# Kernel optimization log

Hardware: AMD Instinct MI355X
Metric: run time of the kernel (lower is better)

The kernel has to match this reference:

```python
import jax, jax.numpy as jnp
import numpy as np

D_MODEL, D_STATE, D_CONV, EXPAND = 1024, 16, 4, 2
D_INNER = EXPAND * D_MODEL
B, L = 2, 4096
LN_EPS = 1e-5


def setup_inputs() -> dict:
    key = jax.random.key(0)
    ks = jax.random.split(key, 6)
    x = jax.random.normal(ks[0], (B, L, D_MODEL), dtype=jnp.float32)
    ln_gamma = jnp.ones((D_MODEL,), jnp.float32)
    ln_beta = jnp.zeros((D_MODEL,), jnp.float32)
    W_in = jax.random.normal(ks[1], (2 * D_INNER, D_MODEL), jnp.float32) / np.sqrt(D_MODEL).astype(np.float32)
    conv_w = jax.random.normal(ks[2], (D_INNER, 1, D_CONV), jnp.float32) * 0.1
    conv_b = jnp.zeros((D_INNER,), jnp.float32)
    W_out = jax.random.normal(ks[3], (D_MODEL, D_INNER), jnp.float32) / np.sqrt(D_INNER).astype(np.float32)
    A = jnp.eye(D_STATE, dtype=jnp.float32)
    Bm = jax.random.normal(ks[4], (D_STATE, D_INNER), jnp.float32) * 0.01
    Cm = jax.random.normal(ks[5], (D_STATE, D_INNER), jnp.float32) * 0.01
    return dict(x=x, ln_gamma=ln_gamma, ln_beta=ln_beta, W_in=W_in,
                conv_w=conv_w, conv_b=conv_b, W_out=W_out, A=A, Bm=Bm, Cm=Cm)


def _layernorm(x, gamma, beta):
    mu = jnp.mean(x, axis=-1, keepdims=True)
    var = jnp.mean(jnp.square(x - mu), axis=-1, keepdims=True)
    return (x - mu) * jax.lax.rsqrt(var + LN_EPS) * gamma + beta


def _causal_depthwise_conv(xp, conv_w, conv_b):
    # xp: (B, L, D_INNER) -> torch Conv1d(padding=K-1, groups=C) then slice [:L]
    # == left-pad K-1, valid depthwise conv.
    lhs = jnp.pad(xp.transpose(0, 2, 1), ((0, 0), (0, 0), (D_CONV - 1, 0)))  # (B,C,L+K-1)
    out = jax.lax.conv_general_dilated(
        lhs, conv_w, window_strides=(1,), padding='VALID',
        dimension_numbers=('NCH', 'OIH', 'NCH'), feature_group_count=D_INNER)
    return out.transpose(0, 2, 1) + conv_b  # (B, L, C)


def reference(x, ln_gamma, ln_beta, W_in, conv_w, conv_b, W_out, A, Bm, Cm):
    # scan permutation is identity (untrained optimizer state); masking disabled
    xn = _layernorm(x, ln_gamma, ln_beta)
    xz = jnp.einsum('bld,ed->ble', xn, W_in)          # (B, L, 2*D_INNER)
    x_part, z = jnp.split(xz, 2, axis=-1)             # each (B, L, D_INNER)
    x_conv = jax.nn.silu(_causal_depthwise_conv(x_part, conv_w, conv_b))

    # recurrence: s_t = s_{t-1} @ A.T + u_t @ B.T ; out_t = (x_conv_t + s_t @ C) * sigmoid(z_t)
    u_seq = x_part.transpose(1, 0, 2)                 # (L, B, D_INNER)
    xc_seq = x_conv.transpose(1, 0, 2)
    z_seq = z.transpose(1, 0, 2)

    def step(state, inp):
        u_t, xc_t, z_t = inp
        state = state @ A.T + u_t @ Bm.T              # (B, D_STATE)
        out = (xc_t + state @ Cm) * jax.nn.sigmoid(z_t)
        return state, out

    state0 = jnp.zeros((x.shape[0], D_STATE), x.dtype)
    _, ys = jax.lax.scan(step, state0, (u_seq, xc_seq, z_seq))
    y = ys.transpose(1, 0, 2)                         # (B, L, D_INNER)
    residual = jnp.einsum('bli,di->bld', y, W_out)    # (B, L, D_MODEL)
    return x + residual
```

## Files before the change

### kernel.cpp

```cpp
#include <hip/hip_runtime.h>
#include <hip/hip_bf16.h>
#include <math.h>

#define D_MODEL 1024
#define D_STATE 16
#define D_CONV 4
#define D_INNER 2048
#define BATCH 2
#define SEQ 4096
#define NROW (BATCH * SEQ)
#define LN_EPS 1e-5f

typedef __attribute__((ext_vector_type(8))) short  bf16x8_t;
typedef __attribute__((ext_vector_type(4))) float  f32x4_t;
typedef __attribute__((ext_vector_type(8))) unsigned short u16x8_t;

__device__ inline unsigned short f2bf(float f) {
    unsigned u = __float_as_uint(f);
    u += 0x7fffu + ((u >> 16) & 1u);
    return (unsigned short)(u >> 16);
}
__device__ inline float bf2f(unsigned short u) {
    return __uint_as_float((unsigned)u << 16);
}

#define GLL16(g, l)                                                            \
    __builtin_amdgcn_global_load_lds(                                          \
        (const __attribute__((address_space(1))) void*)(g),                    \
        (__attribute__((address_space(3))) void*)(l), 16, 0, 0)

#define FENCE asm volatile("" ::: "memory")
#define BAR do { FENCE; __builtin_amdgcn_s_barrier(); FENCE; } while (0)

#define CVT_BLOCKS 3088
__global__ __launch_bounds__(256) void pre_kernel(const float* __restrict__ x,
                                                  const float* __restrict__ gamma,
                                                  const float* __restrict__ beta,
                                                  const float* __restrict__ W_in,
                                                  const float* __restrict__ W_out,
                                                  const float* __restrict__ Bm,
                                                  unsigned short* __restrict__ xn,
                                                  unsigned short* __restrict__ Win_bf,
                                                  unsigned short* __restrict__ Wout_bf,
                                                  unsigned short* __restrict__ Bm_bf) {
    __shared__ float red[8];
    const int tid = threadIdx.x;
    if (blockIdx.x < CVT_BLOCKS) {
        const long long g = (long long)(blockIdx.x * 256 + tid) * 8;
        const long long n1 = (long long)2 * D_INNER * D_MODEL;
        const long long n2 = n1 + (long long)D_MODEL * D_INNER;
        const float* src; unsigned short* dst; long long off;
        if (g < n1)      { src = W_in;  dst = Win_bf;  off = g; }
        else if (g < n2) { src = W_out; dst = Wout_bf; off = g - n1; }
        else             { src = Bm;    dst = Bm_bf;   off = g - n2; }
        const float4 a = *reinterpret_cast<const float4*>(src + off);
        const float4 b = *reinterpret_cast<const float4*>(src + off + 4);
        u16x8_t p;
        p[0] = f2bf(a.x); p[1] = f2bf(a.y); p[2] = f2bf(a.z); p[3] = f2bf(a.w);
        p[4] = f2bf(b.x); p[5] = f2bf(b.y); p[6] = f2bf(b.z); p[7] = f2bf(b.w);
        *reinterpret_cast<u16x8_t*>(dst + off) = p;
        return;
    }
    const int row = blockIdx.x - CVT_BLOCKS;
    const float4* xr = reinterpret_cast<const float4*>(x + (size_t)row * D_MODEL);
    float4 v = xr[tid];

    const int lane = tid & 63, wave = tid >> 6;
    float s = v.x + v.y + v.z + v.w;
    #pragma unroll
    for (int off = 32; off > 0; off >>= 1) s += __shfl_down(s, off, 64);
    if (lane == 0) red[wave] = s;
    __syncthreads();
    float mu = (red[0] + red[1] + red[2] + red[3]) * (1.0f / D_MODEL);
    __syncthreads();

    float dx = v.x - mu, dy = v.y - mu, dz = v.z - mu, dw = v.w - mu;
    float ss = dx * dx + dy * dy + dz * dz + dw * dw;
    #pragma unroll
    for (int off = 32; off > 0; off >>= 1) ss += __shfl_down(ss, off, 64);
    if (lane == 0) red[wave] = ss;
    __syncthreads();
    float var = (red[0] + red[1] + red[2] + red[3]) * (1.0f / D_MODEL);
    float rs = rsqrtf(var + LN_EPS);

    const float4 gv = reinterpret_cast<const float4*>(gamma)[tid];
    const float4 bv = reinterpret_cast<const float4*>(beta)[tid];
    ushort4 o;
    o.x = f2bf(dx * rs * gv.x + bv.x);
    o.y = f2bf(dy * rs * gv.y + bv.y);
    o.z = f2bf(dz * rs * gv.z + bv.z);
    o.w = f2bf(dw * rs * gv.w + bv.w);
    reinterpret_cast<ushort4*>(xn + (size_t)row * D_MODEL)[tid] = o;
}

__global__ __launch_bounds__(512, 2) void gemm256_bf16(const short* __restrict__ A,
                                                       const short* __restrict__ B,
                                                       unsigned short* __restrict__ Cb,
                                                       int M, int N, int K) {
    __shared__ short lds[2 * 4 * 8192];

    const int tid = threadIdx.x;
    const int w = tid >> 6, l = tid & 63;

    const int id = blockIdx.y * gridDim.x + blockIdx.x;
    const int cpx = (gridDim.x * gridDim.y) >> 3;
    const int sid = (id & 7) * cpx + (id >> 3);
    const int row0 = (sid / gridDim.x) * 256;
    const int col0 = (sid % gridDim.x) * 256;

    const int wm = w >> 2;
    const int wn = w & 3;
    const int fr = l & 15;
    const int fc = (l >> 4) * 8;
    const int NT = K >> 6;

    const int qa = wm;
    const int qb = 2 + (wn >> 1);
    const int bb = (wn & 1) * 64;

    auto STAGE = [&](const short* __restrict__ G, int growbase, int k0,
                     int buf, int q) {
        #pragma unroll
        for (int j = 0; j < 2; ++j) {
            const int e = ((j * 8 + w) << 9) + l * 8;
            const int r = e >> 6;
            const int c = (e & 63) ^ ((r & 7) << 3);
            GLL16(G + (size_t)(growbase + r) * K + k0 + c,
                  &lds[buf * 32768 + q * 8192 + ((j * 8 + w) << 9)]);
        }
    };
    auto LDF = [&](int buf, int q, int r, int ks) -> bf16x8_t {
        const int c = (ks * 32 + fc) ^ ((r & 7) << 3);
        return *reinterpret_cast<const bf16x8_t*>(
            &lds[buf * 32768 + q * 8192 + r * 64 + c]);
    };

    f32x4_t acc[8][4] = {};
    bf16x8_t af[4][2], af2[4][2], bA[2][2], bB[2][2];

#define MFMA_Q(AF, mh, nh, BFR)                                                \
    do {                                                                       \
        _Pragma("unroll")                                                      \
        for (int mi = 0; mi < 4; ++mi)                                         \
            _Pragma("unroll")                                                  \
            for (int ni = 0; ni < 2; ++ni)                                     \
                _Pragma("unroll")                                              \
                for (int ks = 0; ks < 2; ++ks)                                 \
                    acc[(mh) * 4 + mi][(nh) * 2 + ni] =                        \
                        __builtin_amdgcn_mfma_f32_16x16x32_bf16(               \
                            AF[mi][ks], BFR[ni][ks],                           \
                            acc[(mh) * 4 + mi][(nh) * 2 + ni], 0, 0, 0);       \
    } while (0)

    STAGE(A, row0,       0, 0, 0);
    STAGE(A, row0 + 128, 0, 0, 1);
    STAGE(B, col0,       0, 0, 2);
    STAGE(B, col0 + 128, 0, 0, 3);
    if (NT > 1) {
        STAGE(B, col0,       64, 1, 2);
        STAGE(B, col0 + 128, 64, 1, 3);
        STAGE(A, row0,       64, 1, 0);
        asm volatile("s_waitcnt vmcnt(6)" ::: "memory");
    } else {
        asm volatile("s_waitcnt vmcnt(0)" ::: "memory");
    }
    BAR;

    for (int kt = 0; kt < NT; ++kt) {
        const int buf = kt & 1, nbuf = buf ^ 1;
        #pragma unroll
        for (int mi = 0; mi < 4; ++mi)
            #pragma unroll
            for (int ks = 0; ks < 2; ++ks)
                af[mi][ks] = LDF(buf, qa, mi * 16 + fr, ks);
        #pragma unroll
        for (int ni = 0; ni < 2; ++ni)
            #pragma unroll
            for (int ks = 0; ks < 2; ++ks)
                bA[ni][ks] = LDF(buf, qb, bb + ni * 16 + fr, ks);
        #pragma unroll
        for (int ni = 0; ni < 2; ++ni)
            #pragma unroll
            for (int ks = 0; ks < 2; ++ks)
                bB[ni][ks] = LDF(buf, qb, bb + 32 + ni * 16 + fr, ks);
        #pragma unroll
        for (int mi = 0; mi < 4; ++mi)
            #pragma unroll
            for (int ks = 0; ks < 2; ++ks)
                af2[mi][ks] = LDF(buf, qa, 64 + mi * 16 + fr, ks);
        if (kt + 1 < NT) STAGE(A, row0 + 128, (kt + 1) << 6, nbuf, 1);
        asm volatile("s_waitcnt lgkmcnt(0)" ::: "memory");
        BAR;
        if (kt + 2 < NT) {
            STAGE(B, col0,       (kt + 2) << 6, buf, 2);
            STAGE(B, col0 + 128, (kt + 2) << 6, buf, 3);
            STAGE(A, row0,       (kt + 2) << 6, buf, 0);
            asm volatile("s_waitcnt vmcnt(6)" ::: "memory");
        } else {
            asm volatile("s_waitcnt vmcnt(0)" ::: "memory");
        }
        BAR;
        __builtin_amdgcn_s_setprio(1);
        MFMA_Q(af,  0, 0, bA);
        MFMA_Q(af,  0, 1, bB);
        MFMA_Q(af2, 1, 1, bB);
        MFMA_Q(af2, 1, 0, bA);
        __builtin_amdgcn_s_setprio(0);
    }
#undef MFMA_Q

    const int cr = (l >> 4) * 4;
    const int cc = l & 15;
    #pragma unroll
    for (int m = 0; m < 8; ++m) {
        #pragma unroll
        for (int n = 0; n < 4; ++n) {
            size_t base = (size_t)(row0 + wm * 128 + m * 16 + cr) * N +
                          (col0 + wn * 64 + n * 16 + cc);
            #pragma unroll
            for (int j = 0; j < 4; ++j)
                Cb[base + (size_t)j * N] = f2bf(acc[m][n][j]);
        }
    }
}

__global__ __launch_bounds__(512) void gemm_out(const short* __restrict__ A,
                                                const short* __restrict__ B,
                                                const float* __restrict__ add,
                                                float* __restrict__ C,
                                                int M, int N, int K) {
    __shared__ short lds[3 * 3 * 8192];

    const int tid = threadIdx.x;
    const int w = tid >> 6, l = tid & 63;

    const int id = blockIdx.y * gridDim.x + blockIdx.x;
    const int cpx = (gridDim.x * gridDim.y) >> 3;
    const int sid = (id & 7) * cpx + (id >> 3);
    const int row0 = (sid / gridDim.x) * 256;
    const int col0 = (sid % gridDim.x) * 128;

    const int wm = w >> 1;
    const int wn = w & 1;
    const int qa = wm >> 1;
    const int lr0 = (wm & 1) * 64;
    const int fr = l & 15;
    const int fc = (l >> 4) * 8;
    const int NT = K >> 6;

    auto STAGE = [&](const short* __restrict__ G, int growbase, int k0,
                     int buf, int q) {
        #pragma unroll
        for (int j = 0; j < 2; ++j) {
            const int e = ((j * 8 + w) << 9) + l * 8;
            const int r = e >> 6;
            const int c = (e & 63) ^ ((r & 7) << 3);
            GLL16(G + (size_t)(growbase + r) * K + k0 + c,
                  &lds[buf * 24576 + q * 8192 + ((j * 8 + w) << 9)]);
        }
    };
    auto LDF = [&](int buf, int q, int r, int ks) -> bf16x8_t {
        const int c = (ks * 32 + fc) ^ ((r & 7) << 3);
        return *reinterpret_cast<const bf16x8_t*>(
            &lds[buf * 24576 + q * 8192 + r * 64 + c]);
    };

    f32x4_t acc[4][4] = {};
    bf16x8_t af[4][2], bf[4][2];

    STAGE(A, row0,       0, 0, 0);
    STAGE(A, row0 + 128, 0, 0, 1);
    STAGE(B, col0,       0, 0, 2);
    if (NT > 1) {
        STAGE(A, row0,       64, 1, 0);
        STAGE(A, row0 + 128, 64, 1, 1);
        STAGE(B, col0,       64, 1, 2);
        asm volatile("s_waitcnt vmcnt(6)" ::: "memory");
    } else {
        asm volatile("s_waitcnt vmcnt(0)" ::: "memory");
    }

    int buf = 0;
    for (int kt = 0; kt < NT; ++kt) {
        BAR;
        #pragma unroll
        for (int mi = 0; mi < 4; ++mi)
            #pragma unroll
            for (int ks = 0; ks < 2; ++ks)
                af[mi][ks] = LDF(buf, qa, lr0 + mi * 16 + fr, ks);
        #pragma unroll
        for (int ni = 0; ni < 4; ++ni)
            #pragma unroll
            for (int ks = 0; ks < 2; ++ks)
                bf[ni][ks] = LDF(buf, 2, wn * 64 + ni * 16 + fr, ks);
        __builtin_amdgcn_s_setprio(1);
        #pragma unroll
        for (int mi = 0; mi < 4; ++mi)
            #pragma unroll
            for (int ni = 0; ni < 4; ++ni)
                #pragma unroll
                for (int ks = 0; ks < 2; ++ks)
                    acc[mi][ni] = __builtin_amdgcn_mfma_f32_16x16x32_bf16(
                        af[mi][ks], bf[ni][ks], acc[mi][ni], 0, 0, 0);
        __builtin_amdgcn_s_setprio(0);
        if (kt + 2 < NT) {
            const int sb = (buf + 2) % 3;
            STAGE(A, row0,       (kt + 2) << 6, sb, 0);
            STAGE(A, row0 + 128, (kt + 2) << 6, sb, 1);
            STAGE(B, col0,       (kt + 2) << 6, sb, 2);
            asm volatile("s_waitcnt vmcnt(6)" ::: "memory");
        } else {
            asm volatile("s_waitcnt vmcnt(0)" ::: "memory");
        }
        buf = (buf + 1) % 3;
    }

    const int cr = (l >> 4) * 4;
    const int cc = l & 15;
    #pragma unroll
    for (int mi = 0; mi < 4; ++mi) {
        #pragma unroll
        for (int ni = 0; ni < 4; ++ni) {
            size_t base = (size_t)(row0 + wm * 64 + mi * 16 + cr) * N +
                          (col0 + wn * 64 + ni * 16 + cc);
            #pragma unroll
            for (int j = 0; j < 4; ++j)
                C[base + (size_t)j * N] = acc[mi][ni][j] + add[base + (size_t)j * N];
        }
    }
}

__global__ __launch_bounds__(128) void v_mfma(const unsigned short* __restrict__ xz,
                                              const unsigned short* __restrict__ Bmb,
                                              float* __restrict__ V) {
    __shared__ float part[2][16][16];
    const int tid = threadIdx.x;
    const int wv = tid >> 6;
    const int l = tid & 63;
    const int r0 = blockIdx.x * 16;
    const int fr = l & 15;
    const int fk = (l >> 4) * 8;
    const int kbase = wv * (D_INNER / 2);

    const unsigned short* aP = xz + (size_t)(r0 + fr) * (2 * D_INNER) + kbase + fk;
    const unsigned short* bP = Bmb + fr * D_INNER + kbase + fk;

    f32x4_t a0 = {}, a1 = {}, a2 = {}, a3 = {};
    #pragma unroll 2
    for (int k0 = 0; k0 < D_INNER / 2; k0 += 128) {
        a0 = __builtin_amdgcn_mfma_f32_16x16x32_bf16(
            *reinterpret_cast<const bf16x8_t*>(aP + k0),
            *reinterpret_cast<const bf16x8_t*>(bP + k0), a0, 0, 0, 0);
        a1 = __builtin_amdgcn_mfma_f32_16x16x32_bf16(
            *reinterpret_cast<const bf16x8_t*>(aP + k0 + 32),
            *reinterpret_cast<const bf16x8_t*>(bP + k0 + 32), a1, 0, 0, 0);
        a2 = __builtin_amdgcn_mfma_f32_16x16x32_bf16(
            *reinterpret_cast<const bf16x8_t*>(aP + k0 + 64),
            *reinterpret_cast<const bf16x8_t*>(bP + k0 + 64), a2, 0, 0, 0);
        a3 = __builtin_amdgcn_mfma_f32_16x16x32_bf16(
            *reinterpret_cast<const bf16x8_t*>(aP + k0 + 96),
            *reinterpret_cast<const bf16x8_t*>(bP + k0 + 96), a3, 0, 0, 0);
    }

    const int cr = (l >> 4) * 4;
    const int cc = l & 15;
    #pragma unroll
    for (int j = 0; j < 4; ++j)
        part[wv][cr + j][cc] = a0[j] + a1[j] + a2[j] + a3[j];
    __syncthreads();
    if (tid < 64) {
        #pragma unroll
        for (int j = 0; j < 4; ++j)
            V[(size_t)(r0 + cr + j) * D_STATE + cc] =
                part[0][cr + j][cc] + part[1][cr + j][cc];
    }
}

#define SCAN_CHUNK 256
__global__ __launch_bounds__(256) void scan_fused(const float* __restrict__ V,
                                                  const float* __restrict__ A,
                                                  float* __restrict__ S) {
    const int tid = threadIdx.x;
    __shared__ int nid;
    if (blockIdx.x < 32) {
        if (tid == 0) nid = 0;
        __syncthreads();
        {
            const float ex = ((tid >> 4) == (tid & 15)) ? 1.0f : 0.0f;
            if (A[tid] != ex) atomicOr(&nid, 1);
        }
        __syncthreads();
        if (nid) return;

        const int p = blockIdx.x;
        const int b = p >> 4, s = p & 15;
        const float* vb = V + (size_t)b * SEQ * D_STATE + s;
        float* sb = S + (size_t)b * SEQ * D_STATE + s;

        const int t0 = tid * 16;
        float v[16];
        float run = 0.0f;
        #pragma unroll
        for (int j = 0; j < 16; ++j) {
            run += vb[(size_t)(t0 + j) * D_STATE];
            v[j] = run;
        }

        const float tot = run;
        float sc = tot;
        #pragma unroll
        for (int off = 1; off < 64; off <<= 1) {
            float n = __shfl_up(sc, off, 64);
            if ((tid & 63) >= off) sc += n;
        }
        __shared__ float wtot[4];
        if ((tid & 63) == 63) wtot[tid >> 6] = sc;
        __syncthreads();
        float woff = 0.0f;
        #pragma unroll
        for (int w2 = 0; w2 < 4; ++w2)
            if (w2 < (tid >> 6)) woff += wtot[w2];
        const float excl = sc - tot + woff;

        #pragma unroll
        for (int j = 0; j < 16; ++j)
            sb[(size_t)(t0 + j) * D_STATE] = v[j] + excl;
        return;
    }

    if (tid == 0) nid = 0;
    __syncthreads();
    {
        const float ex = ((tid >> 4) == (tid & 15)) ? 1.0f : 0.0f;
        if (A[tid] != ex) atomicOr(&nid, 1);
    }
    __syncthreads();
    if (nid == 0) return;

    __shared__ float Al[D_STATE * D_STATE];
    __shared__ float Vl[2 * SCAN_CHUNK * D_STATE];
    __shared__ float Sl[2 * SCAN_CHUNK * D_STATE];

    Al[tid] = A[tid];
    __syncthreads();

    float st = 0.0f;
    const int bb = (tid >> 4) & 1;
    const int ss = tid & 15;

    for (int t0 = 0; t0 < SEQ; t0 += SCAN_CHUNK) {
        for (int idx = tid; idx < 2 * SCAN_CHUNK * D_STATE; idx += 256) {
            int b = idx >> 12;
            int rem = idx & 4095;
            Vl[idx] = V[((size_t)(b * SEQ + t0) * D_STATE) + rem];
        }
        __syncthreads();

        if (tid < 32) {
            float* vb = Vl + bb * SCAN_CHUNK * D_STATE + ss;
            float* sb = Sl + bb * SCAN_CHUNK * D_STATE + ss;
            for (int t = 0; t < SCAN_CHUNK; ++t) {
                float ns = vb[t * D_STATE];
                #pragma unroll
                for (int s2 = 0; s2 < D_STATE; ++s2) {
                    float other = __shfl(st, (tid & 16) | s2, 64);
                    ns = fmaf(Al[ss * D_STATE + s2], other, ns);
                }
                st = ns;
                sb[t * D_STATE] = st;
            }
        }
        __syncthreads();

        for (int idx = tid; idx < 2 * SCAN_CHUNK * D_STATE; idx += 256) {
            int b = idx >> 12;
            int rem = idx & 4095;
            S[((size_t)(b * SEQ + t0) * D_STATE) + rem] = Sl[idx];
        }
        __syncthreads();
    }
}

__global__ __launch_bounds__(256) void y_kernel(const unsigned short* __restrict__ xz,
                                                const float* __restrict__ S,
                                                const float* __restrict__ Cm,
                                                const float* __restrict__ convw,
                                                const float* __restrict__ convb,
                                                unsigned short* __restrict__ y) {
    const int tid = threadIdx.x;
    const int i0 = blockIdx.x * 512 + tid * 2;
    const int r0 = blockIdx.y * 64;
    const int tb0 = r0 & (SEQ - 1);

    const float4 w0 = *reinterpret_cast<const float4*>(&convw[i0 * D_CONV]);
    const float4 w1 = *reinterpret_cast<const float4*>(&convw[(i0 + 1) * D_CONV]);
    const float cb0 = convb[i0], cb1 = convb[i0 + 1];
    float cm0[D_STATE], cm1[D_STATE];
    #pragma unroll
    for (int s = 0; s < D_STATE; ++s) {
        float2 c = *reinterpret_cast<const float2*>(&Cm[s * D_INNER + i0]);
        cm0[s] = c.x; cm1[s] = c.y;
    }

    float2 xm1 = make_float2(0.f, 0.f), xm2 = xm1, xm3 = xm1;
    if (tb0 >= 1) { ushort2 u = *reinterpret_cast<const ushort2*>(&xz[(size_t)(r0 - 1) * (2 * D_INNER) + i0]); xm1 = make_float2(bf2f(u.x), bf2f(u.y)); }
    if (tb0 >= 2) { ushort2 u = *reinterpret_cast<const ushort2*>(&xz[(size_t)(r0 - 2) * (2 * D_INNER) + i0]); xm2 = make_float2(bf2f(u.x), bf2f(u.y)); }
    if (tb0 >= 3) { ushort2 u = *reinterpret_cast<const ushort2*>(&xz[(size_t)(r0 - 3) * (2 * D_INNER) + i0]); xm3 = make_float2(bf2f(u.x), bf2f(u.y)); }

    for (int r = r0; r < r0 + 64; ++r) {
        const ushort2 xu = *reinterpret_cast<const ushort2*>(&xz[(size_t)r * (2 * D_INNER) + i0]);
        const ushort2 zu = *reinterpret_cast<const ushort2*>(&xz[(size_t)r * (2 * D_INNER) + D_INNER + i0]);
        const float2 x0 = make_float2(bf2f(xu.x), bf2f(xu.y));

        float a0 = cb0;
        a0 = fmaf(w0.x, xm3.x, a0); a0 = fmaf(w0.y, xm2.x, a0);
        a0 = fmaf(w0.z, xm1.x, a0); a0 = fmaf(w0.w, x0.x, a0);
        float a1 = cb1;
        a1 = fmaf(w1.x, xm3.y, a1); a1 = fmaf(w1.y, xm2.y, a1);
        a1 = fmaf(w1.z, xm1.y, a1); a1 = fmaf(w1.w, x0.y, a1);

        const float xc0 = a0 / (1.0f + expf(-a0));
        const float xc1 = a1 / (1.0f + expf(-a1));

        const float4* Sp = reinterpret_cast<const float4*>(S + (size_t)r * D_STATE);
        const float4 s0 = Sp[0], s1 = Sp[1], s2 = Sp[2], s3 = Sp[3];
        const float sv[D_STATE] = {s0.x, s0.y, s0.z, s0.w, s1.x, s1.y, s1.z, s1.w,
                                   s2.x, s2.y, s2.z, s2.w, s3.x, s3.y, s3.z, s3.w};
        float sc0 = 0.f, sc1 = 0.f;
        #pragma unroll
        for (int s = 0; s < D_STATE; ++s) {
            sc0 = fmaf(sv[s], cm0[s], sc0);
            sc1 = fmaf(sv[s], cm1[s], sc1);
        }

        const float z0 = bf2f(zu.x), z1 = bf2f(zu.y);
        const float g0 = 1.0f / (1.0f + expf(-z0));
        const float g1 = 1.0f / (1.0f + expf(-z1));

        ushort2 o;
        o.x = f2bf((xc0 + sc0) * g0);
        o.y = f2bf((xc1 + sc1) * g1);
        *reinterpret_cast<ushort2*>(&y[(size_t)r * D_INNER + i0]) = o;

        xm3 = xm2; xm2 = xm1; xm1 = x0;
    }
}

extern "C" void kernel_launch(void* const* d_in, const int* in_sizes, int n_in,
                              void* d_out, int out_size, void* d_ws, size_t ws_size,
                              hipStream_t stream) {
    const float* x      = (const float*)d_in[0];
    const float* ln_g   = (const float*)d_in[1];
    const float* ln_b   = (const float*)d_in[2];
    const float* W_in   = (const float*)d_in[3];
    const float* conv_w = (const float*)d_in[4];
    const float* conv_b = (const float*)d_in[5];
    const float* W_out  = (const float*)d_in[6];
    const float* A      = (const float*)d_in[7];
    const float* Bm     = (const float*)d_in[8];
    const float* Cm     = (const float*)d_in[9];
    float* out = (float*)d_out;

    float* ws = (float*)d_ws;
    float* V  = ws;
    float* S  = V + (size_t)NROW * D_STATE;
    unsigned short* xz_bf  = (unsigned short*)(S + (size_t)NROW * D_STATE);
    unsigned short* xn_bf  = xz_bf  + (size_t)NROW * 2 * D_INNER;
    unsigned short* Win_bf = xn_bf  + (size_t)NROW * D_MODEL;
    unsigned short* Wout_bf= Win_bf + (size_t)(2 * D_INNER) * D_MODEL;
    unsigned short* Bm_bf  = Wout_bf + (size_t)D_MODEL * D_INNER;
    unsigned short* y_bf   = Bm_bf  + (size_t)D_STATE * D_INNER;

    pre_kernel<<<CVT_BLOCKS + NROW, 256, 0, stream>>>(
        x, ln_g, ln_b, W_in, W_out, Bm, xn_bf, Win_bf, Wout_bf, Bm_bf);

    gemm256_bf16<<<dim3((2 * D_INNER) / 256, NROW / 256), 512, 0, stream>>>(
        (const short*)xn_bf, (const short*)Win_bf, xz_bf,
        NROW, 2 * D_INNER, D_MODEL);

    v_mfma<<<NROW / 16, 128, 0, stream>>>(xz_bf, Bm_bf, V);

    scan_fused<<<33, 256, 0, stream>>>(V, A, S);

    y_kernel<<<dim3(D_INNER / 512, NROW / 64), 256, 0, stream>>>(
        xz_bf, S, Cm, conv_w, conv_b, y_bf);

    gemm_out<<<dim3(D_MODEL / 128, NROW / 256), 512, 0, stream>>>(
        (const short*)y_bf, (const short*)Wout_bf, x, out,
        NROW, D_MODEL, D_INNER);
}
```

Baseline: 187.6 us.

## Move W_out/Bm conversion into first GEMM launch and software-pipeline output GEMM

The W_out and Bm fp32-to-bf16 conversion moves out of the pre-kernel and into extra tail blocks of the first GEMM launch. The first GEMM grid becomes 1D with hardcoded tile swizzling. This shortens the pre-kernel's critical path and lets the conversion fill idle CUs while the GEMM runs. The output GEMM now uses double-buffered register fragments so LDS reads for the next k-tile overlap the current MFMAs, at the cost of more registers, and it adds a 2-blocks-per-CU launch bound that may not fit with 3-stage LDS.

New measurement: 189.3 us. Within noise of the previous version (+0.9%).

```diff
diff --git a/kernel.cpp b/kernel.cpp
--- a/kernel.cpp
+++ b/kernel.cpp
@@ -32,33 +32,23 @@
 #define FENCE asm volatile("" ::: "memory")
 #define BAR do { FENCE; __builtin_amdgcn_s_barrier(); FENCE; } while (0)
 
-#define CVT_BLOCKS 3088
+#define CVT_BLOCKS 2048
 __global__ __launch_bounds__(256) void pre_kernel(const float* __restrict__ x,
                                                   const float* __restrict__ gamma,
                                                   const float* __restrict__ beta,
                                                   const float* __restrict__ W_in,
-                                                  const float* __restrict__ W_out,
-                                                  const float* __restrict__ Bm,
                                                   unsigned short* __restrict__ xn,
-                                                  unsigned short* __restrict__ Win_bf,
-                                                  unsigned short* __restrict__ Wout_bf,
-                                                  unsigned short* __restrict__ Bm_bf) {
+                                                  unsigned short* __restrict__ Win_bf) {
     __shared__ float red[8];
     const int tid = threadIdx.x;
     if (blockIdx.x < CVT_BLOCKS) {
-        const long long g = (long long)(blockIdx.x * 256 + tid) * 8;
-        const long long n1 = (long long)2 * D_INNER * D_MODEL;
-        const long long n2 = n1 + (long long)D_MODEL * D_INNER;
-        const float* src; unsigned short* dst; long long off;
-        if (g < n1)      { src = W_in;  dst = Win_bf;  off = g; }
-        else if (g < n2) { src = W_out; dst = Wout_bf; off = g - n1; }
-        else             { src = Bm;    dst = Bm_bf;   off = g - n2; }
-        const float4 a = *reinterpret_cast<const float4*>(src + off);
-        const float4 b = *reinterpret_cast<const float4*>(src + off + 4);
+        const long long off = (long long)(blockIdx.x * 256 + tid) * 8;
+        const float4 a = *reinterpret_cast<const float4*>(W_in + off);
+        const float4 b = *reinterpret_cast<const float4*>(W_in + off + 4);
         u16x8_t p;
         p[0] = f2bf(a.x); p[1] = f2bf(a.y); p[2] = f2bf(a.z); p[3] = f2bf(a.w);
         p[4] = f2bf(b.x); p[5] = f2bf(b.y); p[6] = f2bf(b.z); p[7] = f2bf(b.w);
-        *reinterpret_cast<u16x8_t*>(dst + off) = p;
+        *reinterpret_cast<u16x8_t*>(Win_bf + off) = p;
         return;
     }
     const int row = blockIdx.x - CVT_BLOCKS;
@@ -93,20 +83,39 @@
     reinterpret_cast<ushort4*>(xn + (size_t)row * D_MODEL)[tid] = o;
 }
 
+#define G1_BLOCKS 512
 __global__ __launch_bounds__(512, 2) void gemm256_bf16(const short* __restrict__ A,
                                                        const short* __restrict__ B,
                                                        unsigned short* __restrict__ Cb,
+                                                       const float* __restrict__ W_out,
+                                                       const float* __restrict__ Bm,
+                                                       unsigned short* __restrict__ Wout_bf,
+                                                       unsigned short* __restrict__ Bm_bf,
                                                        int M, int N, int K) {
     __shared__ short lds[2 * 4 * 8192];
 
     const int tid = threadIdx.x;
+    if (blockIdx.x >= G1_BLOCKS) {
+        const long long g = (long long)(blockIdx.x - G1_BLOCKS) * 4096 + tid * 8;
+        const long long n1 = (long long)D_MODEL * D_INNER;
+        const float* src; unsigned short* dst; long long off;
+        if (g < n1) { src = W_out; dst = Wout_bf; off = g; }
+        else        { src = Bm;    dst = Bm_bf;   off = g - n1; }
+        const float4 a = *reinterpret_cast<const float4*>(src + off);
+        const float4 b = *reinterpret_cast<const float4*>(src + off + 4);
+        u16x8_t p;
+        p[0] = f2bf(a.x); p[1] = f2bf(a.y); p[2] = f2bf(a.z); p[3] = f2bf(a.w);
+        p[4] = f2bf(b.x); p[5] = f2bf(b.y); p[6] = f2bf(b.z); p[7] = f2bf(b.w);
+        *reinterpret_cast<u16x8_t*>(dst + off) = p;
+        return;
+    }
+
     const int w = tid >> 6, l = tid & 63;
 
-    const int id = blockIdx.y * gridDim.x + blockIdx.x;
-    const int cpx = (gridDim.x * gridDim.y) >> 3;
-    const int sid = (id & 7) * cpx + (id >> 3);
-    const int row0 = (sid / gridDim.x) * 256;
-    const int col0 = (sid % gridDim.x) * 256;
+    const int id = blockIdx.x;
+    const int sid = (id & 7) * 64 + (id >> 3);
+    const int row0 = (sid >> 4) * 256;
+    const int col0 = (sid & 15) * 256;
 
     const int wm = w >> 2;
     const int wn = w & 3;
@@ -224,11 +233,11 @@
     }
 }
 
-__global__ __launch_bounds__(512) void gemm_out(const short* __restrict__ A,
-                                                const short* __restrict__ B,
-                                                const float* __restrict__ add,
-                                                float* __restrict__ C,
-                                                int M, int N, int K) {
+__global__ __launch_bounds__(512, 2) void gemm_out(const short* __restrict__ A,
+                                                   const short* __restrict__ B,
+                                                   const float* __restrict__ add,
+                                                   float* __restrict__ C,
+                                                   int M, int N, int K) {
     __shared__ short lds[3 * 3 * 8192];
 
     const int tid = threadIdx.x;
@@ -266,7 +275,36 @@
     };
 
     f32x4_t acc[4][4] = {};
-    bf16x8_t af[4][2], bf[4][2];
+    bf16x8_t afA[4][2], bfA[4][2];
+    bf16x8_t afB[4][2], bfB[4][2];
+
+#define READS(AF, BF, rb)                                                      \
+    do {                                                                       \
+        _Pragma("unroll")                                                      \
+        for (int mi = 0; mi < 4; ++mi)                                         \
+            _Pragma("unroll")                                                  \
+            for (int ks = 0; ks < 2; ++ks)                                     \
+                AF[mi][ks] = LDF(rb, qa, lr0 + mi * 16 + fr, ks);              \
+        _Pragma("unroll")                                                      \
+        for (int ni = 0; ni < 4; ++ni)                                         \
+            _Pragma("unroll")                                                  \
+            for (int ks = 0; ks < 2; ++ks)                                     \
+                BF[ni][ks] = LDF(rb, 2, wn * 64 + ni * 16 + fr, ks);           \
+    } while (0)
+
+#define MFMAS(AF, BF)                                                          \
+    do {                                                                       \
+        __builtin_amdgcn_s_setprio(1);                                         \
+        _Pragma("unroll")                                                      \
+        for (int mi = 0; mi < 4; ++mi)                                         \
+            _Pragma("unroll")                                                  \
+            for (int ni = 0; ni < 4; ++ni)                                     \
+                _Pragma("unroll")                                              \
+                for (int ks = 0; ks < 2; ++ks)                                 \
+                    acc[mi][ni] = __builtin_amdgcn_mfma_f32_16x16x32_bf16(     \
+                        AF[mi][ks], BF[ni][ks], acc[mi][ni], 0, 0, 0);         \
+        __builtin_amdgcn_s_setprio(0);                                         \
+    } while (0)
 
     STAGE(A, row0,       0, 0, 0);
     STAGE(A, row0 + 128, 0, 0, 1);
@@ -275,45 +313,44 @@
         STAGE(A, row0,       64, 1, 0);
         STAGE(A, row0 + 128, 64, 1, 1);
         STAGE(B, col0,       64, 1, 2);
-        asm volatile("s_waitcnt vmcnt(6)" ::: "memory");
-    } else {
-        asm volatile("s_waitcnt vmcnt(0)" ::: "memory");
-    }
+    }
+    asm volatile("s_waitcnt vmcnt(0)" ::: "memory");
+    BAR;
+    READS(afA, bfA, 0);
 
     int buf = 0;
-    for (int kt = 0; kt < NT; ++kt) {
-        BAR;
-        #pragma unroll
-        for (int mi = 0; mi < 4; ++mi)
-            #pragma unroll
-            for (int ks = 0; ks < 2; ++ks)
-                af[mi][ks] = LDF(buf, qa, lr0 + mi * 16 + fr, ks);
-        #pragma unroll
-        for (int ni = 0; ni < 4; ++ni)
-            #pragma unroll
-            for (int ks = 0; ks < 2; ++ks)
-                bf[ni][ks] = LDF(buf, 2, wn * 64 + ni * 16 + fr, ks);
-        __builtin_amdgcn_s_setprio(1);
-        #pragma unroll
-        for (int mi = 0; mi < 4; ++mi)
-            #pragma unroll
-            for (int ni = 0; ni < 4; ++ni)
-                #pragma unroll
-                for (int ks = 0; ks < 2; ++ks)
-                    acc[mi][ni] = __builtin_amdgcn_mfma_f32_16x16x32_bf16(
-                        af[mi][ks], bf[ni][ks], acc[mi][ni], 0, 0, 0);
-        __builtin_amdgcn_s_setprio(0);
-        if (kt + 2 < NT) {
-            const int sb = (buf + 2) % 3;
-            STAGE(A, row0,       (kt + 2) << 6, sb, 0);
-            STAGE(A, row0 + 128, (kt + 2) << 6, sb, 1);
-            STAGE(B, col0,       (kt + 2) << 6, sb, 2);
-            asm volatile("s_waitcnt vmcnt(6)" ::: "memory");
-        } else {
+    for (int kt = 0; kt < NT; kt += 2) {
+        {
+            const int sb = buf + 2 >= 3 ? buf - 1 : buf + 2;
+            const int rb = buf + 1 >= 3 ? buf - 2 : buf + 1;
+            if (kt + 2 < NT) {
+                STAGE(A, row0,       (kt + 2) << 6, sb, 0);
+                STAGE(A, row0 + 128, (kt + 2) << 6, sb, 1);
+                STAGE(B, col0,       (kt + 2) << 6, sb, 2);
+            }
+            if (kt + 1 < NT) READS(afB, bfB, rb);
+            MFMAS(afA, bfA);
             asm volatile("s_waitcnt vmcnt(0)" ::: "memory");
-        }
-        buf = (buf + 1) % 3;
-    }
+            BAR;
+            buf = rb;
+        }
+        if (kt + 1 < NT) {
+            const int sb = buf + 2 >= 3 ? buf - 1 : buf + 2;
+            const int rb = buf + 1 >= 3 ? buf - 2 : buf + 1;
+            if (kt + 3 < NT) {
+                STAGE(A, row0,       (kt + 3) << 6, sb, 0);
+                STAGE(A, row0 + 128, (kt + 3) << 6, sb, 1);
+                STAGE(B, col0,       (kt + 3) << 6, sb, 2);
+            }
+            if (kt + 2 < NT) READS(afA, bfA, rb);
+            MFMAS(afB, bfB);
+            asm volatile("s_waitcnt vmcnt(0)" ::: "memory");
+            BAR;
+            buf = rb;
+        }
+    }
+#undef READS
+#undef MFMAS
 
     const int cr = (l >> 4) * 4;
     const int cc = l & 15;
@@ -572,10 +609,11 @@
     unsigned short* y_bf   = Bm_bf  + (size_t)D_STATE * D_INNER;
 
     pre_kernel<<<CVT_BLOCKS + NROW, 256, 0, stream>>>(
-        x, ln_g, ln_b, W_in, W_out, Bm, xn_bf, Win_bf, Wout_bf, Bm_bf);
-
-    gemm256_bf16<<<dim3((2 * D_INNER) / 256, NROW / 256), 512, 0, stream>>>(
+        x, ln_g, ln_b, W_in, xn_bf, Win_bf);
+
+    gemm256_bf16<<<G1_BLOCKS + 520, 512, 0, stream>>>(
         (const short*)xn_bf, (const short*)Win_bf, xz_bf,
+        W_out, Bm, Wout_bf, Bm_bf,
         NROW, 2 * D_INNER, D_MODEL);
 
     v_mfma<<<NROW / 16, 128, 0, stream>>>(xz_bf, Bm_bf, V);
```
